# Optimization experiments

Measured on AMD Instinct MI355X. Metric: run time of the kernel, lower is better.

The kernel has to match this reference:

```python
import jax, jax.numpy as jnp
import numpy as np

B, IN, OUT, Q = 2048, 1024, 1024, 16

def setup_inputs() -> dict:
    key = jax.random.key(0)
    k1, k2, k3, k4 = jax.random.split(key, 4)
    bound = 1.0 / np.sqrt(IN)
    x = jax.random.normal(k1, (B, IN), dtype=jnp.float32)
    indices = jax.random.randint(k2, (B, IN), 0, Q, dtype=jnp.int32)
    # param_index: per-(quantile, input-feature) weight vector of length size_out
    param_table = jax.random.uniform(k3, (Q, IN, OUT), dtype=jnp.float32,
                                     minval=-bound, maxval=bound)
    bias = jax.random.uniform(k4, (OUT,), dtype=jnp.float32,
                              minval=-bound, maxval=bound)
    return {"x": x, "indices": indices, "param_table": param_table,
            "bias": bias, "store_activations": 0, "get_indices": 0, "use_db": 0}

def reference(x, indices, param_table, bias, store_activations, get_indices, use_db):
    # out[b, o] = sum_i param_table[indices[b,i], i, o] * x[b,i]  + bias[o]
    # Expressed as Q masked matmuls to avoid a [B, IN, OUT] gathered intermediate:
    # route each (b, i) contribution to its quantile's weight slab.
    q = param_table.shape[0]
    onehot = jax.nn.one_hot(indices, q, dtype=x.dtype)      # [B, IN, Q]
    xq = onehot * x[..., None]                               # [B, IN, Q]
    w_times_x = jnp.einsum('biq,qio->bo', xq, param_table)   # [B, OUT]
    return w_times_x + bias
```

## Files before the change

### kernel.cpp

```cpp
#include <hip/hip_runtime.h>
#include <stdint.h>

#define B_SZ   2048
#define IN_SZ  1024
#define OUT_SZ 1024
#define Q_SZ   16
#define NZB    4

typedef __attribute__((ext_vector_type(8))) short short8;
typedef __attribute__((ext_vector_type(4))) float floatx4;
typedef __attribute__((ext_vector_type(2))) unsigned short u16x2;

__device__ __forceinline__ unsigned short f32_to_bf16_rne(float f) {
    union { float f; uint32_t u; } v; v.f = f;
    uint32_t u = v.u;
    return (unsigned short)((u + 0x7FFFu + ((u >> 16) & 1u)) >> 16);
}

__device__ __forceinline__ uint32_t mask2(uint32_t xv, uint32_t iv, uint32_t qq) {
    union { uint32_t u; u16x2 v; } t, m;
    t.u = iv ^ qq;
    u16x2 one; one.x = 1; one.y = 1;
    m.v = __builtin_elementwise_min(t.v, one) - one;
    return xv & m.u;
}

__global__ void k_build_wf(const float* __restrict__ W, unsigned short* __restrict__ Wf) {
    const int S = blockIdx.x;
    const int q  = S & 15, ih = (S >> 4) & 3, xb = (S >> 6) & 7, zb = S >> 9;
    const int t = threadIdx.x;
    unsigned short* dst = Wf + (size_t)S * 8192;
#pragma unroll
    for (int it = 0; it < 4; ++it) {
        int c = it * 256 + t;
        int L = c & 63;
        int hnt = c >> 6;
        int h = hnt >> 3, nt = hnt & 7;
        int o  = xb * 128 + nt * 16 + (L & 15);
        int i0 = zb * 256 + ih * 64 + h * 32 + (L >> 4) * 8;
        const float* src = W + ((size_t)(q * 1024 + i0)) * 1024 + o;
        unsigned short v[8];
#pragma unroll
        for (int j = 0; j < 8; ++j) v[j] = f32_to_bf16_rne(src[(size_t)j * 1024]);
        *(uint4*)(dst + (size_t)c * 8) = *(uint4*)v;
    }
}

__global__ __launch_bounds__(256, 2) void k_gemm(const unsigned short* __restrict__ Wf,
                                                 const float* __restrict__ x,
                                                 const int* __restrict__ idx,
                                                 float* __restrict__ P) {
    const int tid  = threadIdx.x;
    const int wave = tid >> 6, lane = tid & 63;

    const int id = blockIdx.x;
    const int zb = id & 3;
    const int xb = (id >> 2) & 7;
    const int yb = id >> 5;
    const int o0 = xb * 128, b0 = yb * 128, ibase = zb * 256;

    const char* wbase = (const char*)Wf + (size_t)(zb * 8 + xb) * 64 * 16384;
    const int   lofs  = lane * 16;

    const int arow = b0 + wave * 32 + (lane & 15);
    const float* xg = x + (size_t)arow * IN_SZ + ibase + (lane >> 4) * 8;
    const int*   ig = idx + (size_t)arow * IN_SZ + ibase + (lane >> 4) * 8;

    floatx4 acc[16];
#pragma unroll
    for (int i = 0; i < 16; ++i) acc[i] = (floatx4){0.f, 0.f, 0.f, 0.f};

    uint4 xr[2][2], ir[2][2];
    short8 bA[8], bB[8];

#define LOADB(d, s, h)                                                        \
    {   const char* p_ = wbase + (size_t)(s) * 16384 + (h) * 8192 + lofs;     \
        _Pragma("unroll")                                                     \
        for (int nt_ = 0; nt_ < 8; ++nt_)                                     \
            (d)[nt_] = *(const short8*)(p_ + nt_ * 1024);                     \
    }

#define RELOADA(ih)                                                           \
    {   int io_ = (ih) * 64;                                                  \
        _Pragma("unroll")                                                     \
        for (int mt_ = 0; mt_ < 2; ++mt_)                                     \
            _Pragma("unroll")                                                 \
            for (int hh_ = 0; hh_ < 2; ++hh_) {                               \
                const float* xp_ = xg + mt_ * 16 * IN_SZ + io_ + hh_ * 32;    \
                const int*   ip_ = ig + mt_ * 16 * IN_SZ + io_ + hh_ * 32;    \
                float a_[8]; int b_[8];                                       \
                *(float4*)(a_)     = *(const float4*)xp_;                     \
                *(float4*)(a_ + 4) = *((const float4*)xp_ + 1);               \
                *(int4*)(b_)       = *(const int4*)ip_;                       \
                *(int4*)(b_ + 4)   = *((const int4*)ip_ + 1);                 \
                unsigned short xv_[8];                                        \
                _Pragma("unroll")                                             \
                for (int j_ = 0; j_ < 8; ++j_) xv_[j_] = f32_to_bf16_rne(a_[j_]); \
                xr[mt_][hh_] = *(uint4*)xv_;                                  \
                uint32_t iw_[4];                                              \
                _Pragma("unroll")                                             \
                for (int w_ = 0; w_ < 4; ++w_)                                \
                    iw_[w_] = ((uint32_t)b_[2 * w_] & 0xFFFFu) |              \
                              ((uint32_t)b_[2 * w_ + 1] << 16);               \
                ir[mt_][hh_] = *(uint4*)iw_;                                  \
            }                                                                 \
    }

    RELOADA(0);
    LOADB(bA, 0, 0);

    for (int s = 0; s < 64; ++s) {
        if (s && (s & 15) == 0) RELOADA(s >> 4);
        LOADB(bB, s, 1);
        const uint32_t qq = (uint32_t)(s & 15) * 0x00010001u;

        union { uint4 u; short8 s8; } aF[2];
#pragma unroll
        for (int mt = 0; mt < 2; ++mt) {
            aF[mt].u.x = mask2(xr[mt][0].x, ir[mt][0].x, qq);
            aF[mt].u.y = mask2(xr[mt][0].y, ir[mt][0].y, qq);
            aF[mt].u.z = mask2(xr[mt][0].z, ir[mt][0].z, qq);
            aF[mt].u.w = mask2(xr[mt][0].w, ir[mt][0].w, qq);
        }
#pragma unroll
        for (int mt = 0; mt < 2; ++mt)
#pragma unroll
            for (int nt = 0; nt < 8; ++nt)
                acc[mt * 8 + nt] = __builtin_amdgcn_mfma_f32_16x16x32_bf16(
                    aF[mt].s8, bA[nt], acc[mt * 8 + nt], 0, 0, 0);

        if (s < 63) LOADB(bA, s + 1, 0);

#pragma unroll
        for (int mt = 0; mt < 2; ++mt) {
            aF[mt].u.x = mask2(xr[mt][1].x, ir[mt][1].x, qq);
            aF[mt].u.y = mask2(xr[mt][1].y, ir[mt][1].y, qq);
            aF[mt].u.z = mask2(xr[mt][1].z, ir[mt][1].z, qq);
            aF[mt].u.w = mask2(xr[mt][1].w, ir[mt][1].w, qq);
        }
#pragma unroll
        for (int mt = 0; mt < 2; ++mt)
#pragma unroll
            for (int nt = 0; nt < 8; ++nt)
                acc[mt * 8 + nt] = __builtin_amdgcn_mfma_f32_16x16x32_bf16(
                    aF[mt].s8, bB[nt], acc[mt * 8 + nt], 0, 0, 0);
    }

    float* Pz = P + (size_t)zb * (B_SZ * OUT_SZ);
    int cn = lane & 15, rq = lane >> 4;
#pragma unroll
    for (int mt = 0; mt < 2; ++mt)
#pragma unroll
        for (int nt = 0; nt < 8; ++nt) {
            int bb = b0 + wave * 32 + mt * 16 + rq * 4;
            int oo = o0 + nt * 16 + cn;
#pragma unroll
            for (int e = 0; e < 4; ++e)
                Pz[(size_t)(bb + e) * OUT_SZ + oo] = acc[mt * 8 + nt][e];
        }
#undef LOADB
#undef RELOADA
}

__global__ void k_reduce(const float* __restrict__ P, const float* __restrict__ bias,
                         float* __restrict__ out) {
    int t = blockIdx.x * 256 + threadIdx.x;
    const float4* b4 = (const float4*)bias;
    float4 a = b4[t & 255];
#pragma unroll
    for (int z = 0; z < NZB; ++z) {
        float4 v = ((const float4*)P)[(size_t)z * (B_SZ * OUT_SZ / 4) + t];
        a.x += v.x; a.y += v.y; a.z += v.z; a.w += v.w;
    }
    ((float4*)out)[t] = a;
}

__global__ void k_naive(const float* __restrict__ x, const int* __restrict__ idx,
                        const float* __restrict__ W, const float* __restrict__ bias,
                        float* __restrict__ out) {
    int b = blockIdx.x;
    int o = threadIdx.x * 4;
    float4 acc = *(const float4*)(bias + o);
    const float* xr = x + (size_t)b * IN_SZ;
    const int*   ir = idx + (size_t)b * IN_SZ;
    for (int i = 0; i < IN_SZ; ++i) {
        float xv = xr[i];
        int q = ir[i];
        float4 w4 = *(const float4*)(W + ((size_t)q * IN_SZ + i) * OUT_SZ + o);
        acc.x += xv * w4.x; acc.y += xv * w4.y;
        acc.z += xv * w4.z; acc.w += xv * w4.w;
    }
    *(float4*)(out + (size_t)b * OUT_SZ + o) = acc;
}

extern "C" void kernel_launch(void* const* d_in, const int* in_sizes, int n_in,
                              void* d_out, int out_size, void* d_ws, size_t ws_size,
                              hipStream_t stream) {
    const float* x    = (const float*)d_in[0];
    const int*   idx  = (const int*)d_in[1];
    const float* W    = (const float*)d_in[2];
    const float* bias = (const float*)d_in[3];
    float* out = (float*)d_out;

    const size_t wf_bytes = (size_t)2048 * 16384;
    const size_t p_bytes  = (size_t)NZB * B_SZ * OUT_SZ * 4;
    if (ws_size < wf_bytes + p_bytes) {
        k_naive<<<dim3(B_SZ), dim3(256), 0, stream>>>(x, idx, W, bias, out);
        return;
    }
    unsigned short* Wf = (unsigned short*)d_ws;
    float* P = (float*)((char*)d_ws + wf_bytes);

    k_build_wf<<<dim3(2048), dim3(256), 0, stream>>>(W, Wf);
    k_gemm<<<dim3(NZB * 8 * (B_SZ / 128)), dim3(256), 0, stream>>>(Wf, x, idx, P);
    k_reduce<<<dim3(2048), dim3(256), 0, stream>>>(P, bias, out);
}
```

Before: 209.8 us.

## Deepen B prefetch, use one-hot shift masks, stage weight repack via LDS

The GEMM loop now prefetches both halves of the next weight slab a full slab ahead into four rotating register buffers (ping-pong of two slabs), instead of one half ahead. The index mask is precomputed as a one-hot bit per element so each slab's mask is a shift-left and arithmetic shift-right rather than xor/min/sub. The weight repack kernel now reads W with coalesced float4 loads into LDS, then gathers the fragment layout from LDS, replacing strided global reads. The deeper prefetch raises register pressure (32 short8 B registers), which could spill or cut occupancy at launch bounds of 2.

```diff
diff --git a/kernel.cpp b/kernel.cpp
--- a/kernel.cpp
+++ b/kernel.cpp
@@ -10,6 +10,7 @@
 typedef __attribute__((ext_vector_type(8))) short short8;
 typedef __attribute__((ext_vector_type(4))) float floatx4;
 typedef __attribute__((ext_vector_type(2))) unsigned short u16x2;
+typedef __attribute__((ext_vector_type(2))) short s16x2;
 
 __device__ __forceinline__ unsigned short f32_to_bf16_rne(float f) {
     union { float f; uint32_t u; } v; v.f = f;
@@ -17,18 +18,36 @@
     return (unsigned short)((u + 0x7FFFu + ((u >> 16) & 1u)) >> 16);
 }
 
-__device__ __forceinline__ uint32_t mask2(uint32_t xv, uint32_t iv, uint32_t qq) {
-    union { uint32_t u; u16x2 v; } t, m;
-    t.u = iv ^ qq;
-    u16x2 one; one.x = 1; one.y = 1;
-    m.v = __builtin_elementwise_min(t.v, one) - one;
-    return xv & m.u;
+__device__ __forceinline__ uint32_t mask3(uint32_t xv, uint32_t ohv, unsigned short sh) {
+    union { uint32_t u; u16x2 v; s16x2 s; } t;
+    t.u = ohv;
+    u16x2 shv; shv.x = sh; shv.y = sh;
+    t.v = t.v << shv;
+    s16x2 f15; f15.x = 15; f15.y = 15;
+    t.s = t.s >> f15;
+    return xv & t.u;
 }
 
 __global__ void k_build_wf(const float* __restrict__ W, unsigned short* __restrict__ Wf) {
     const int S = blockIdx.x;
-    const int q  = S & 15, ih = (S >> 4) & 3, xb = (S >> 6) & 7, zb = S >> 9;
+    const int q = S & 15, ih = (S >> 4) & 3, xb = (S >> 6) & 7, zb = S >> 9;
     const int t = threadIdx.x;
+    const int i0 = zb * 256 + ih * 64;
+    const int o0 = xb * 128;
+    __shared__ unsigned short lds[64][130];
+
+#pragma unroll
+    for (int it = 0; it < 8; ++it) {
+        int r  = it * 8 + (t >> 5);
+        int c4 = (t & 31) * 4;
+        float4 v = *(const float4*)(W + ((size_t)(q * 1024 + i0 + r)) * 1024 + o0 + c4);
+        unsigned short h0 = f32_to_bf16_rne(v.x), h1 = f32_to_bf16_rne(v.y);
+        unsigned short h2 = f32_to_bf16_rne(v.z), h3 = f32_to_bf16_rne(v.w);
+        *(uint32_t*)&lds[r][c4]     = (uint32_t)h0 | ((uint32_t)h1 << 16);
+        *(uint32_t*)&lds[r][c4 + 2] = (uint32_t)h2 | ((uint32_t)h3 << 16);
+    }
+    __syncthreads();
+
     unsigned short* dst = Wf + (size_t)S * 8192;
 #pragma unroll
     for (int it = 0; it < 4; ++it) {
@@ -36,12 +55,11 @@
         int L = c & 63;
         int hnt = c >> 6;
         int h = hnt >> 3, nt = hnt & 7;
-        int o  = xb * 128 + nt * 16 + (L & 15);
-        int i0 = zb * 256 + ih * 64 + h * 32 + (L >> 4) * 8;
-        const float* src = W + ((size_t)(q * 1024 + i0)) * 1024 + o;
+        int ol = nt * 16 + (L & 15);
+        int il = h * 32 + (L >> 4) * 8;
         unsigned short v[8];
 #pragma unroll
-        for (int j = 0; j < 8; ++j) v[j] = f32_to_bf16_rne(src[(size_t)j * 1024]);
+        for (int j = 0; j < 8; ++j) v[j] = lds[il + j][ol];
         *(uint4*)(dst + (size_t)c * 8) = *(uint4*)v;
     }
 }
@@ -70,8 +88,8 @@
 #pragma unroll
     for (int i = 0; i < 16; ++i) acc[i] = (floatx4){0.f, 0.f, 0.f, 0.f};
 
-    uint4 xr[2][2], ir[2][2];
-    short8 bA[8], bB[8];
+    uint4 xr[2][2], oh[2][2];
+    short8 rb0[8], rb1[8], rb2[8], rb3[8];
 
 #define LOADB(d, s, h)                                                        \
     {   const char* p_ = wbase + (size_t)(s) * 16384 + (h) * 8192 + lofs;     \
@@ -100,50 +118,50 @@
                 uint32_t iw_[4];                                              \
                 _Pragma("unroll")                                             \
                 for (int w_ = 0; w_ < 4; ++w_)                                \
-                    iw_[w_] = ((uint32_t)b_[2 * w_] & 0xFFFFu) |              \
-                              ((uint32_t)b_[2 * w_ + 1] << 16);               \
-                ir[mt_][hh_] = *(uint4*)iw_;                                  \
+                    iw_[w_] = (1u << b_[2 * w_]) | ((1u << b_[2 * w_ + 1]) << 16); \
+                oh[mt_][hh_] = *(uint4*)iw_;                                  \
             }                                                                 \
     }
 
+#define MASKS(hh)                                                             \
+        _Pragma("unroll")                                                     \
+        for (int mt_ = 0; mt_ < 2; ++mt_) {                                   \
+            aF[mt_].u.x = mask3(xr[mt_][hh].x, oh[mt_][hh].x, sh_);           \
+            aF[mt_].u.y = mask3(xr[mt_][hh].y, oh[mt_][hh].y, sh_);           \
+            aF[mt_].u.z = mask3(xr[mt_][hh].z, oh[mt_][hh].z, sh_);           \
+            aF[mt_].u.w = mask3(xr[mt_][hh].w, oh[mt_][hh].w, sh_);           \
+        }
+
+#define SLAB(s_, Bc0, Bc1, Bn0, Bn1)                                          \
+    {   if ((s_) && (((s_) & 15) == 0)) RELOADA((s_) >> 4);                   \
+        if ((s_) < 63) LOADB(Bn0, (s_) + 1, 0);                               \
+        const unsigned short sh_ = (unsigned short)(15 - ((s_) & 15));        \
+        union { uint4 u; short8 s8; } aF[2];                                  \
+        MASKS(0);                                                             \
+        _Pragma("unroll")                                                     \
+        for (int mt_ = 0; mt_ < 2; ++mt_)                                     \
+            _Pragma("unroll")                                                 \
+            for (int nt_ = 0; nt_ < 8; ++nt_)                                 \
+                acc[mt_ * 8 + nt_] = __builtin_amdgcn_mfma_f32_16x16x32_bf16( \
+                    aF[mt_].s8, (Bc0)[nt_], acc[mt_ * 8 + nt_], 0, 0, 0);     \
+        if ((s_) < 63) LOADB(Bn1, (s_) + 1, 1);                               \
+        MASKS(1);                                                             \
+        _Pragma("unroll")                                                     \
+        for (int mt_ = 0; mt_ < 2; ++mt_)                                     \
+            _Pragma("unroll")                                                 \
+            for (int nt_ = 0; nt_ < 8; ++nt_)                                 \
+                acc[mt_ * 8 + nt_] = __builtin_amdgcn_mfma_f32_16x16x32_bf16( \
+                    aF[mt_].s8, (Bc1)[nt_], acc[mt_ * 8 + nt_], 0, 0, 0);     \
+    }
+
     RELOADA(0);
-    LOADB(bA, 0, 0);
-
-    for (int s = 0; s < 64; ++s) {
-        if (s && (s & 15) == 0) RELOADA(s >> 4);
-        LOADB(bB, s, 1);
-        const uint32_t qq = (uint32_t)(s & 15) * 0x00010001u;
-
-        union { uint4 u; short8 s8; } aF[2];
-#pragma unroll
-        for (int mt = 0; mt < 2; ++mt) {
-            aF[mt].u.x = mask2(xr[mt][0].x, ir[mt][0].x, qq);
-            aF[mt].u.y = mask2(xr[mt][0].y, ir[mt][0].y, qq);
-            aF[mt].u.z = mask2(xr[mt][0].z, ir[mt][0].z, qq);
-            aF[mt].u.w = mask2(xr[mt][0].w, ir[mt][0].w, qq);
-        }
-#pragma unroll
-        for (int mt = 0; mt < 2; ++mt)
-#pragma unroll
-            for (int nt = 0; nt < 8; ++nt)
-                acc[mt * 8 + nt] = __builtin_amdgcn_mfma_f32_16x16x32_bf16(
-                    aF[mt].s8, bA[nt], acc[mt * 8 + nt], 0, 0, 0);
-
-        if (s < 63) LOADB(bA, s + 1, 0);
-
-#pragma unroll
-        for (int mt = 0; mt < 2; ++mt) {
-            aF[mt].u.x = mask2(xr[mt][1].x, ir[mt][1].x, qq);
-            aF[mt].u.y = mask2(xr[mt][1].y, ir[mt][1].y, qq);
-            aF[mt].u.z = mask2(xr[mt][1].z, ir[mt][1].z, qq);
-            aF[mt].u.w = mask2(xr[mt][1].w, ir[mt][1].w, qq);
-        }
-#pragma unroll
-        for (int mt = 0; mt < 2; ++mt)
-#pragma unroll
-            for (int nt = 0; nt < 8; ++nt)
-                acc[mt * 8 + nt] = __builtin_amdgcn_mfma_f32_16x16x32_bf16(
-                    aF[mt].s8, bB[nt], acc[mt * 8 + nt], 0, 0, 0);
+    LOADB(rb0, 0, 0);
+    LOADB(rb1, 0, 1);
+
+#pragma unroll 1
+    for (int g = 0; g < 32; ++g) {
+        SLAB(2 * g,     rb0, rb1, rb2, rb3);
+        SLAB(2 * g + 1, rb2, rb3, rb0, rb1);
     }
 
     float* Pz = P + (size_t)zb * (B_SZ * OUT_SZ);
@@ -160,6 +178,8 @@
         }
 #undef LOADB
 #undef RELOADA
+#undef MASKS
+#undef SLAB
 }
 
 __global__ void k_reduce(const float* __restrict__ P, const float* __restrict__ bias,
```

After: 205.7 us. -2.0%, faster.
